# Optimization experiments

Measured on AMD Instinct MI355X. Metric: run time of the kernel, lower is better.

## Reference

```python
import jax, jax.numpy as jnp
import numpy as np

N_SAMPLES, N_NODES, IN_CH, HID, OUT_CH = 262144, 24, 32, 32, 1

def setup_inputs() -> dict:
    key = jax.random.key(0)
    k = jax.random.split(key, 6)
    h = jax.random.normal(k[0], (N_SAMPLES, N_NODES, IN_CH), dtype=jnp.float32)
    valid = jax.random.randint(k[1], (N_SAMPLES, N_NODES), 0, 2, dtype=jnp.int32)
    # per-node MLP params, PyTorch-style init scale ~ 1/sqrt(fan_in)
    W1 = jax.random.normal(k[2], (N_NODES, IN_CH, HID), dtype=jnp.float32) / np.sqrt(IN_CH)
    b1 = jax.random.normal(k[3], (N_NODES, HID), dtype=jnp.float32) / np.sqrt(IN_CH)
    W2 = jax.random.normal(k[4], (N_NODES, HID, OUT_CH), dtype=jnp.float32) / np.sqrt(HID)
    b2 = jax.random.normal(k[5], (N_NODES, OUT_CH), dtype=jnp.float32) / np.sqrt(HID)
    return {"h": h, "valid": valid, "W1": W1, "b1": b1, "W2": W2, "b2": b2}

def reference(h, valid, W1, b1, W2, b2):
    # Per-node MLP: input ReLU -> Linear(in,W) -> ReLU -> Linear(W,out).
    # Instead of a Python loop with gather/scatter over nodes, run all
    # nodes as a batched (grouped) GEMM and mask invalid entries to zero
    # (the torch code leaves invalid slots at their zero init).
    x = jax.nn.relu(h)                                    # [S, N, C]
    x = jax.nn.relu(jnp.einsum('snc,ncw->snw', x, W1) + b1[None])  # [S, N, W]
    out = jnp.einsum('snw,nwo->sno', x, W2) + b2[None]    # [S, N, O]
    mask = (valid > 0)[:, :, None]                        # [S, N, 1]
    return jnp.where(mask, out, jnp.zeros((), out.dtype))
```

## Files before the change

### kernel.cpp

```cpp
#include <hip/hip_runtime.h>

#define NS  262144
#define NN  24
#define CI  32
#define HW  32
#define SPB 16

typedef __fp16 fp16x2v __attribute__((ext_vector_type(2)));
typedef _Float16 half2v __attribute__((ext_vector_type(2)));
typedef _Float16 half8 __attribute__((ext_vector_type(8)));
typedef float f32x4 __attribute__((ext_vector_type(4)));
typedef unsigned int u32x4 __attribute__((ext_vector_type(4)));

__device__ alignas(16) unsigned short g_w1f[NN * 2 * 64 * 8];

__global__ void pack_w1(const float* __restrict__ W1) {
  int idx = blockIdx.x * 256 + threadIdx.x;
  if (idx >= NN * 2 * 64 * 8) return;
  int i    = idx & 7;
  int lane = (idx >> 3) & 63;
  int hf   = (idx >> 9) & 1;
  int n    = idx >> 10;
  int k = (lane >> 4) * 8 + i;
  int w = hf * 16 + (lane & 15);
  _Float16 v = (_Float16)W1[(n * CI + k) * HW + w];
  g_w1f[idx] = __builtin_bit_cast(unsigned short, v);
}

__device__ __forceinline__ unsigned pkrtz(float a, float b) {
#if __has_builtin(__builtin_amdgcn_cvt_pkrtz)
  fp16x2v p = __builtin_amdgcn_cvt_pkrtz(a, b);
  return __builtin_bit_cast(unsigned, p);
#else
  half2v p;
  p[0] = (_Float16)a;
  p[1] = (_Float16)b;
  return __builtin_bit_cast(unsigned, p);
#endif
}

__global__ __launch_bounds__(256, 5) void mlp_mfma(
    const float* __restrict__ h, const int* __restrict__ valid,
    const float* __restrict__ b1, const float* __restrict__ W2,
    const float* __restrict__ b2, float* __restrict__ out) {
  __shared__ alignas(16) unsigned short lds[NN * SPB * CI];

  const int tid = threadIdx.x;
  const int sB  = blockIdx.x * SPB;
  const float* __restrict__ gb = h + (size_t)sB * (NN * CI);

#pragma unroll
  for (int rd = 0; rd < 6; ++rd) {
    const int c32 = rd * 256 + tid;
    const int row = c32 >> 2;
    const int q2  = c32 & 3;
    const int sl  = row / NN;
    const int n   = row - sl * NN;
    const float* hp = gb + (size_t)c32 * 8;
    f32x4 d0 = *(const f32x4*)hp;
    f32x4 d1 = *(const f32x4*)(hp + 4);
    u32x4 u;
    u[0] = pkrtz(fmaxf(d0[0], 0.f), fmaxf(d0[1], 0.f));
    u[1] = pkrtz(fmaxf(d0[2], 0.f), fmaxf(d0[3], 0.f));
    u[2] = pkrtz(fmaxf(d1[0], 0.f), fmaxf(d1[1], 0.f));
    u[3] = pkrtz(fmaxf(d1[2], 0.f), fmaxf(d1[3], 0.f));
    int byte = n * (SPB * CI * 2) + sl * (CI * 2) + q2 * 16;
    byte ^= ((sl ^ n) & 7) << 4;
    *(u32x4*)((char*)lds + byte) = u;
  }
  __syncthreads();

  const int lane = tid & 63;
  const int wv   = tid >> 6;
  const int r    = lane & 15;
  const int q    = lane >> 4;

  for (int ni = 0; ni < 6; ++ni) {
    const int n = wv * 6 + ni;
    half8 Af0 = __builtin_bit_cast(half8,
        *(const u32x4*)&g_w1f[((n * 2 + 0) * 64 + lane) * 8]);
    half8 Af1 = __builtin_bit_cast(half8,
        *(const u32x4*)&g_w1f[((n * 2 + 1) * 64 + lane) * 8]);
    f32x4 b1a = *(const f32x4*)&b1[n * HW + q * 4];
    f32x4 b1b = *(const f32x4*)&b1[n * HW + 16 + q * 4];
    f32x4 w2a = *(const f32x4*)&W2[n * HW + q * 4];
    f32x4 w2b = *(const f32x4*)&W2[n * HW + 16 + q * 4];
    float b2n = b2[n];

    int byte = n * (SPB * CI * 2) + r * (CI * 2) + q * 16;
    byte ^= ((r ^ n) & 7) << 4;
    half8 Hf = *(const half8*)((const char*)lds + byte);

    f32x4 c0 = {b1a[0], b1a[1], b1a[2], b1a[3]};
    f32x4 c1 = {b1b[0], b1b[1], b1b[2], b1b[3]};
    c0 = __builtin_amdgcn_mfma_f32_16x16x32_f16(Af0, Hf, c0, 0, 0, 0);
    c1 = __builtin_amdgcn_mfma_f32_16x16x32_f16(Af1, Hf, c1, 0, 0, 0);

    float p = 0.f;
#pragma unroll
    for (int i = 0; i < 4; ++i) {
      p = fmaf(fmaxf(c0[i], 0.f), w2a[i], p);
      p = fmaf(fmaxf(c1[i], 0.f), w2b[i], p);
    }
    p += __shfl_xor(p, 16);
    p += __shfl_xor(p, 32);

    if (lane < 16) {
      const int srow = sB + r;
      const int vv = valid[srow * NN + n];
      out[(size_t)srow * NN + n] = vv ? (p + b2n) : 0.0f;
    }
  }
}

extern "C" void kernel_launch(void* const* d_in, const int* in_sizes, int n_in,
                              void* d_out, int out_size, void* d_ws, size_t ws_size,
                              hipStream_t stream) {
  const float* h     = (const float*)d_in[0];
  const int*   valid = (const int*)d_in[1];
  const float* W1    = (const float*)d_in[2];
  const float* b1    = (const float*)d_in[3];
  const float* W2    = (const float*)d_in[4];
  const float* b2    = (const float*)d_in[5];
  float* out = (float*)d_out;

  hipLaunchKernelGGL(pack_w1, dim3((NN * 2 * 64 * 8 + 255) / 256), dim3(256),
                     0, stream, W1);
  hipLaunchKernelGGL(mlp_mfma, dim3(NS / SPB), dim3(256), 0, stream,
                     h, valid, b1, W2, b2, out);
}
```

Baseline: 224.1 us.

## Make blocks persistent over eight tiles with double-buffered LDS prefetch

```diff
diff --git a/kernel.cpp b/kernel.cpp
--- a/kernel.cpp
+++ b/kernel.cpp
@@ -5,6 +5,7 @@
 #define CI  32
 #define HW  32
 #define SPB 16
+#define TPB 8
 
 typedef __fp16 fp16x2v __attribute__((ext_vector_type(2)));
 typedef _Float16 half2v __attribute__((ext_vector_type(2)));
@@ -39,77 +40,118 @@
 #endif
 }
 
-__global__ __launch_bounds__(256, 5) void mlp_mfma(
+__global__ __launch_bounds__(256, 3) void mlp_mfma(
     const float* __restrict__ h, const int* __restrict__ valid,
     const float* __restrict__ b1, const float* __restrict__ W2,
     const float* __restrict__ b2, float* __restrict__ out) {
-  __shared__ alignas(16) unsigned short lds[NN * SPB * CI];
+  __shared__ alignas(16) unsigned short lds[2][NN * SPB * CI];
 
-  const int tid = threadIdx.x;
-  const int sB  = blockIdx.x * SPB;
-  const float* __restrict__ gb = h + (size_t)sB * (NN * CI);
-
-#pragma unroll
-  for (int rd = 0; rd < 6; ++rd) {
-    const int c32 = rd * 256 + tid;
-    const int row = c32 >> 2;
-    const int q2  = c32 & 3;
-    const int sl  = row / NN;
-    const int n   = row - sl * NN;
-    const float* hp = gb + (size_t)c32 * 8;
-    f32x4 d0 = *(const f32x4*)hp;
-    f32x4 d1 = *(const f32x4*)(hp + 4);
-    u32x4 u;
-    u[0] = pkrtz(fmaxf(d0[0], 0.f), fmaxf(d0[1], 0.f));
-    u[1] = pkrtz(fmaxf(d0[2], 0.f), fmaxf(d0[3], 0.f));
-    u[2] = pkrtz(fmaxf(d1[0], 0.f), fmaxf(d1[1], 0.f));
-    u[3] = pkrtz(fmaxf(d1[2], 0.f), fmaxf(d1[3], 0.f));
-    int byte = n * (SPB * CI * 2) + sl * (CI * 2) + q2 * 16;
-    byte ^= ((sl ^ n) & 7) << 4;
-    *(u32x4*)((char*)lds + byte) = u;
-  }
-  __syncthreads();
-
+  const int tid  = threadIdx.x;
   const int lane = tid & 63;
   const int wv   = tid >> 6;
   const int r    = lane & 15;
   const int q    = lane >> 4;
+  const int sB   = blockIdx.x * (SPB * TPB);
 
+  half8 Af0[6], Af1[6];
+#pragma unroll
   for (int ni = 0; ni < 6; ++ni) {
     const int n = wv * 6 + ni;
-    half8 Af0 = __builtin_bit_cast(half8,
+    Af0[ni] = __builtin_bit_cast(half8,
         *(const u32x4*)&g_w1f[((n * 2 + 0) * 64 + lane) * 8]);
-    half8 Af1 = __builtin_bit_cast(half8,
+    Af1[ni] = __builtin_bit_cast(half8,
         *(const u32x4*)&g_w1f[((n * 2 + 1) * 64 + lane) * 8]);
-    f32x4 b1a = *(const f32x4*)&b1[n * HW + q * 4];
-    f32x4 b1b = *(const f32x4*)&b1[n * HW + 16 + q * 4];
-    f32x4 w2a = *(const f32x4*)&W2[n * HW + q * 4];
-    f32x4 w2b = *(const f32x4*)&W2[n * HW + 16 + q * 4];
-    float b2n = b2[n];
+  }
 
-    int byte = n * (SPB * CI * 2) + r * (CI * 2) + q * 16;
-    byte ^= ((r ^ n) & 7) << 4;
-    half8 Hf = *(const half8*)((const char*)lds + byte);
+  f32x4 ra[6], rb[6];
 
-    f32x4 c0 = {b1a[0], b1a[1], b1a[2], b1a[3]};
-    f32x4 c1 = {b1b[0], b1b[1], b1b[2], b1b[3]};
-    c0 = __builtin_amdgcn_mfma_f32_16x16x32_f16(Af0, Hf, c0, 0, 0, 0);
-    c1 = __builtin_amdgcn_mfma_f32_16x16x32_f16(Af1, Hf, c1, 0, 0, 0);
+#pragma unroll
+  for (int rd = 0; rd < 6; ++rd) {
+    const float* hp = h + (size_t)sB * (NN * CI) + (size_t)(rd * 256 + tid) * 8;
+    ra[rd] = *(const f32x4*)hp;
+    rb[rd] = *(const f32x4*)(hp + 4);
+  }
+#pragma unroll
+  for (int rd = 0; rd < 6; ++rd) {
+    const int c32 = rd * 256 + tid;
+    const int row = c32 >> 2, q2 = c32 & 3;
+    const int sl  = row / NN, n = row - sl * NN;
+    u32x4 u;
+    u[0] = pkrtz(fmaxf(ra[rd][0], 0.f), fmaxf(ra[rd][1], 0.f));
+    u[1] = pkrtz(fmaxf(ra[rd][2], 0.f), fmaxf(ra[rd][3], 0.f));
+    u[2] = pkrtz(fmaxf(rb[rd][0], 0.f), fmaxf(rb[rd][1], 0.f));
+    u[3] = pkrtz(fmaxf(rb[rd][2], 0.f), fmaxf(rb[rd][3], 0.f));
+    int byte = n * (SPB * CI * 2) + sl * (CI * 2) + q2 * 16;
+    byte ^= ((sl ^ n) & 7) << 4;
+    *(u32x4*)((char*)lds[0] + byte) = u;
+  }
+  __syncthreads();
 
-    float p = 0.f;
+  for (int t = 0; t < TPB; ++t) {
+    const int p = t & 1;
+
+    if (t + 1 < TPB) {
+      const float* gbt = h + (size_t)(sB + (t + 1) * SPB) * (NN * CI);
 #pragma unroll
-    for (int i = 0; i < 4; ++i) {
-      p = fmaf(fmaxf(c0[i], 0.f), w2a[i], p);
-      p = fmaf(fmaxf(c1[i], 0.f), w2b[i], p);
+      for (int rd = 0; rd < 6; ++rd) {
+        const float* hp = gbt + (size_t)(rd * 256 + tid) * 8;
+        ra[rd] = *(const f32x4*)hp;
+        rb[rd] = *(const f32x4*)(hp + 4);
+      }
     }
-    p += __shfl_xor(p, 16);
-    p += __shfl_xor(p, 32);
 
-    if (lane < 16) {
-      const int srow = sB + r;
-      const int vv = valid[srow * NN + n];
-      out[(size_t)srow * NN + n] = vv ? (p + b2n) : 0.0f;
+    const int sBt = sB + t * SPB;
+#pragma unroll
+    for (int ni = 0; ni < 6; ++ni) {
+      const int n = wv * 6 + ni;
+      f32x4 b1a = *(const f32x4*)&b1[n * HW + q * 4];
+      f32x4 b1b = *(const f32x4*)&b1[n * HW + 16 + q * 4];
+      f32x4 w2a = *(const f32x4*)&W2[n * HW + q * 4];
+      f32x4 w2b = *(const f32x4*)&W2[n * HW + 16 + q * 4];
+      float b2n = b2[n];
+
+      int byte = n * (SPB * CI * 2) + r * (CI * 2) + q * 16;
+      byte ^= ((r ^ n) & 7) << 4;
+      half8 Hf = *(const half8*)((const char*)lds[p] + byte);
+
+      f32x4 c0 = {b1a[0], b1a[1], b1a[2], b1a[3]};
+      f32x4 c1 = {b1b[0], b1b[1], b1b[2], b1b[3]};
+      c0 = __builtin_amdgcn_mfma_f32_16x16x32_f16(Af0[ni], Hf, c0, 0, 0, 0);
+      c1 = __builtin_amdgcn_mfma_f32_16x16x32_f16(Af1[ni], Hf, c1, 0, 0, 0);
+
+      float pacc = 0.f;
+#pragma unroll
+      for (int i = 0; i < 4; ++i) {
+        pacc = fmaf(fmaxf(c0[i], 0.f), w2a[i], pacc);
+        pacc = fmaf(fmaxf(c1[i], 0.f), w2b[i], pacc);
+      }
+      pacc += __shfl_xor(pacc, 16);
+      pacc += __shfl_xor(pacc, 32);
+
+      if (lane < 16) {
+        const int srow = sBt + r;
+        const int vv = valid[srow * NN + n];
+        out[(size_t)srow * NN + n] = vv ? (pacc + b2n) : 0.0f;
+      }
     }
+
+    if (t + 1 < TPB) {
+#pragma unroll
+      for (int rd = 0; rd < 6; ++rd) {
+        const int c32 = rd * 256 + tid;
+        const int row = c32 >> 2, q2 = c32 & 3;
+        const int sl  = row / NN, n = row - sl * NN;
+        u32x4 u;
+        u[0] = pkrtz(fmaxf(ra[rd][0], 0.f), fmaxf(ra[rd][1], 0.f));
+        u[1] = pkrtz(fmaxf(ra[rd][2], 0.f), fmaxf(ra[rd][3], 0.f));
+        u[2] = pkrtz(fmaxf(rb[rd][0], 0.f), fmaxf(rb[rd][1], 0.f));
+        u[3] = pkrtz(fmaxf(rb[rd][2], 0.f), fmaxf(rb[rd][3], 0.f));
+        int byte = n * (SPB * CI * 2) + sl * (CI * 2) + q2 * 16;
+        byte ^= ((sl ^ n) & 7) << 4;
+        *(u32x4*)((char*)lds[p ^ 1] + byte) = u;
+      }
+    }
+    __syncthreads();
   }
 }
 
@@ -126,6 +168,6 @@
 
   hipLaunchKernelGGL(pack_w1, dim3((NN * 2 * 64 * 8 + 255) / 256), dim3(256),
                      0, stream, W1);
-  hipLaunchKernelGGL(mlp_mfma, dim3(NS / SPB), dim3(256), 0, stream,
+  hipLaunchKernelGGL(mlp_mfma, dim3(NS / (SPB * TPB)), dim3(256), 0, stream,
                      h, valid, b1, W2, b2, out);
 }
```

After: 368.2 us. 1.64x slower.

## Load activations directly into MFMA fragments, stage biases and W2 in LDS

Applied to the files above, without the earlier changes.

```diff
diff --git a/kernel.cpp b/kernel.cpp
--- a/kernel.cpp
+++ b/kernel.cpp
@@ -4,7 +4,6 @@
 #define NN  24
 #define CI  32
 #define HW  32
-#define SPB 16
 
 typedef __fp16 fp16x2v __attribute__((ext_vector_type(2)));
 typedef _Float16 half2v __attribute__((ext_vector_type(2)));
@@ -39,34 +38,22 @@
 #endif
 }
 
-__global__ __launch_bounds__(256, 5) void mlp_mfma(
+__global__ __launch_bounds__(256, 4) void mlp_mfma(
     const float* __restrict__ h, const int* __restrict__ valid,
     const float* __restrict__ b1, const float* __restrict__ W2,
     const float* __restrict__ b2, float* __restrict__ out) {
-  __shared__ alignas(16) unsigned short lds[NN * SPB * CI];
+  __shared__ float sb1[NN * HW];
+  __shared__ float sw2[NN * HW];
+  __shared__ float sb2[NN];
 
   const int tid = threadIdx.x;
-  const int sB  = blockIdx.x * SPB;
-  const float* __restrict__ gb = h + (size_t)sB * (NN * CI);
-
-#pragma unroll
-  for (int rd = 0; rd < 6; ++rd) {
-    const int c32 = rd * 256 + tid;
-    const int row = c32 >> 2;
-    const int q2  = c32 & 3;
-    const int sl  = row / NN;
-    const int n   = row - sl * NN;
-    const float* hp = gb + (size_t)c32 * 8;
-    f32x4 d0 = *(const f32x4*)hp;
-    f32x4 d1 = *(const f32x4*)(hp + 4);
-    u32x4 u;
-    u[0] = pkrtz(fmaxf(d0[0], 0.f), fmaxf(d0[1], 0.f));
-    u[1] = pkrtz(fmaxf(d0[2], 0.f), fmaxf(d0[3], 0.f));
-    u[2] = pkrtz(fmaxf(d1[0], 0.f), fmaxf(d1[1], 0.f));
-    u[3] = pkrtz(fmaxf(d1[2], 0.f), fmaxf(d1[3], 0.f));
-    int byte = n * (SPB * CI * 2) + sl * (CI * 2) + q2 * 16;
-    byte ^= ((sl ^ n) & 7) << 4;
-    *(u32x4*)((char*)lds + byte) = u;
+  {
+    const int t4 = tid * 4;
+    if (t4 < NN * HW) {
+      *(f32x4*)&sb1[t4] = *(const f32x4*)&b1[t4];
+      *(f32x4*)&sw2[t4] = *(const f32x4*)&W2[t4];
+    }
+    if (tid < NN) sb2[tid] = b2[tid];
   }
   __syncthreads();
 
@@ -74,22 +61,34 @@
   const int wv   = tid >> 6;
   const int r    = lane & 15;
   const int q    = lane >> 4;
+  const int s0   = blockIdx.x * 64 + wv * 16;
+  const int srow = s0 + r;
 
-  for (int ni = 0; ni < 6; ++ni) {
-    const int n = wv * 6 + ni;
+  const float* __restrict__ hbase = h + (size_t)srow * (NN * CI) + q * 8;
+
+#pragma unroll 4
+  for (int n = 0; n < NN; ++n) {
+    const int vld = valid[srow * NN + n];
+    const float* hp = hbase + n * CI;
+    f32x4 av0 = *(const f32x4*)hp;
+    f32x4 av1 = *(const f32x4*)(hp + 4);
+
     half8 Af0 = __builtin_bit_cast(half8,
         *(const u32x4*)&g_w1f[((n * 2 + 0) * 64 + lane) * 8]);
     half8 Af1 = __builtin_bit_cast(half8,
         *(const u32x4*)&g_w1f[((n * 2 + 1) * 64 + lane) * 8]);
-    f32x4 b1a = *(const f32x4*)&b1[n * HW + q * 4];
-    f32x4 b1b = *(const f32x4*)&b1[n * HW + 16 + q * 4];
-    f32x4 w2a = *(const f32x4*)&W2[n * HW + q * 4];
-    f32x4 w2b = *(const f32x4*)&W2[n * HW + 16 + q * 4];
-    float b2n = b2[n];
+    f32x4 b1a = *(const f32x4*)&sb1[n * HW + q * 4];
+    f32x4 b1b = *(const f32x4*)&sb1[n * HW + 16 + q * 4];
+    f32x4 w2a = *(const f32x4*)&sw2[n * HW + q * 4];
+    f32x4 w2b = *(const f32x4*)&sw2[n * HW + 16 + q * 4];
+    const float b2n = sb2[n];
 
-    int byte = n * (SPB * CI * 2) + r * (CI * 2) + q * 16;
-    byte ^= ((r ^ n) & 7) << 4;
-    half8 Hf = *(const half8*)((const char*)lds + byte);
+    u32x4 uu;
+    uu[0] = pkrtz(fmaxf(av0[0], 0.f), fmaxf(av0[1], 0.f));
+    uu[1] = pkrtz(fmaxf(av0[2], 0.f), fmaxf(av0[3], 0.f));
+    uu[2] = pkrtz(fmaxf(av1[0], 0.f), fmaxf(av1[1], 0.f));
+    uu[3] = pkrtz(fmaxf(av1[2], 0.f), fmaxf(av1[3], 0.f));
+    half8 Hf = __builtin_bit_cast(half8, uu);
 
     f32x4 c0 = {b1a[0], b1a[1], b1a[2], b1a[3]};
     f32x4 c1 = {b1b[0], b1b[1], b1b[2], b1b[3]};
@@ -105,11 +104,8 @@
     p += __shfl_xor(p, 16);
     p += __shfl_xor(p, 32);
 
-    if (lane < 16) {
-      const int srow = sB + r;
-      const int vv = valid[srow * NN + n];
-      out[(size_t)srow * NN + n] = vv ? (p + b2n) : 0.0f;
-    }
+    if (lane < 16)
+      out[(size_t)srow * NN + n] = vld ? (p + b2n) : 0.0f;
   }
 }
 
@@ -126,6 +122,6 @@
 
   hipLaunchKernelGGL(pack_w1, dim3((NN * 2 * 64 * 8 + 255) / 256), dim3(256),
                      0, stream, W1);
-  hipLaunchKernelGGL(mlp_mfma, dim3(NS / SPB), dim3(256), 0, stream,
+  hipLaunchKernelGGL(mlp_mfma, dim3(NS / 64), dim3(256), 0, stream,
                      h, valid, b1, W2, b2, out);
 }
```

Result: slower. 295.2 us (+31.7%).
